# Optimization experiments

Hardware: AMD Instinct MI355X
Metric: run time of the kernel (lower is better)

Reference implementation:

```python
import jax, jax.numpy as jnp
import numpy as np

ALPHA = 0.25
GAMMA = 2.0
EPS = 1e-8
COST_CLASS_W = 1.0
COST_KP_W = 1.0


def setup_inputs() -> dict:
    key = jax.random.key(0)
    k1, k2, k3 = jax.random.split(key, 3)
    bs, nq, num_classes, T, D = 16, 1024, 2, 64, 63
    pred_logits = jax.random.normal(k1, (bs, nq, num_classes), dtype=jnp.float32)
    pred_keypoints = jax.random.normal(k2, (bs, nq, D), dtype=jnp.float32)
    tgt_kp = jax.random.normal(k3, (T, D), dtype=jnp.float32)  # ~half > 0 -> occlusion mask
    tgt_ids = jnp.ones((T,), dtype=jnp.int64)  # all 'hand' class; hand_idx all True
    return {"pred_logits": pred_logits, "pred_keypoints": pred_keypoints,
            "tgt_kp": tgt_kp, "tgt_ids": tgt_ids}


def reference(pred_logits, pred_keypoints, tgt_kp, tgt_ids):
    bs, nq, _ = pred_logits.shape
    out_prob = jax.nn.sigmoid(pred_logits.reshape(bs * nq, -1))   # [Q, C]
    out_kp = pred_keypoints.reshape(bs * nq, -1)                  # [Q, 63]

    # Focal-style classification cost
    neg = (1.0 - ALPHA) * out_prob ** GAMMA * (-jnp.log1p(-(out_prob - EPS) - 1.0 + 1.0) if False else -jnp.log(1.0 - out_prob + EPS))
    pos = ALPHA * (1.0 - out_prob) ** GAMMA * (-jnp.log(out_prob + EPS))
    cost_class = pos[:, tgt_ids] - neg[:, tgt_ids]                # [Q, T]

    # Masked L1 'cdist': only visible (tgt_kp > 0) coordinates contribute.
    occl_mask = (tgt_kp > 0).astype(out_kp.dtype)                 # [T, 63]
    diff = jnp.abs(out_kp[:, None, :] - tgt_kp[None, :, :])       # [Q, T, 63]
    cost_kp = jnp.sum(diff * occl_mask[None, :, :], axis=-1)      # [Q, T]

    C = COST_KP_W * cost_kp + COST_CLASS_W * cost_class
    return C.reshape(bs, nq, -1)  # [bs, nq, T]; CPU Hungarian (scipy) consumes per-sample blocks
```

## Files before the change

### kernel.cpp

```cpp
#include <hip/hip_runtime.h>


#define ALPHA 0.25f
#define EPS 1e-8f

constexpr int Q  = 16 * 1024;
constexpr int T  = 64;
constexpr int D  = 63;
constexpr int QB = 64;
constexpr int P  = 68;
constexpr int P2 = 34;

__device__ inline float focal_cost(float x) {
  float p   = 1.0f / (1.0f + __expf(-x));
  float pos = ALPHA * (1.0f - p) * (1.0f - p) * (-__logf(p + EPS));
  float neg = (1.0f - ALPHA) * p * p * (-__logf(1.0f - p + EPS));
  return pos - neg;
}

__global__ __launch_bounds__(512) void matcher_kernel(
    const float* __restrict__ logits,
    const float* __restrict__ kp,
    const float* __restrict__ tgt,
    const int*   __restrict__ ids,
    float* __restrict__ out)
{
  __shared__ __align__(16) float Bv[64 * P];
  __shared__ __align__(16) float Bm[64 * P];
  __shared__ float Lcc[QB * 2];
  __shared__ int   Ids[T];

  const int tid   = threadIdx.x;
  const int qbase = blockIdx.x * QB;

  {
    const float4* src = (const float4*)tgt;
    for (int j = tid; j < T * D / 4; j += 512) {
      float4 v = src[j];
      int i0 = 4 * j;
      float vv[4] = {v.x, v.y, v.z, v.w};
#pragma unroll
      for (int c = 0; c < 4; ++c) {
        int idx = i0 + c;
        int t = idx / D;
        int d = idx - t * D;
        Bv[d * P + t] = vv[c];
        Bm[d * P + t] = (vv[c] > 0.0f) ? 1.0f : 0.0f;
      }
    }
  }
  if (tid < QB * 2) Lcc[tid] = focal_cost(logits[qbase * 2 + tid]);
  if (tid < T) Ids[tid] = ids[tid];
  __syncthreads();

  const int qg = tid >> 5;
  const int tg = tid & 31;

  const float* __restrict__ r0 = kp + (qbase + qg * 4 + 0) * D;
  const float* __restrict__ r1 = kp + (qbase + qg * 4 + 1) * D;
  const float* __restrict__ r2 = kp + (qbase + qg * 4 + 2) * D;
  const float* __restrict__ r3 = kp + (qbase + qg * 4 + 3) * D;

  float2 acc0 = make_float2(0.f, 0.f);
  float2 acc1 = acc0, acc2 = acc0, acc3 = acc0;

  const float2* Bv2 = (const float2*)Bv;
  const float2* Bm2 = (const float2*)Bm;

#pragma unroll 7
  for (int d = 0; d < D; ++d) {
    float a0 = r0[d], a1 = r1[d], a2 = r2[d], a3 = r3[d];
    float2 bv = Bv2[d * P2 + tg];
    float2 bm = Bm2[d * P2 + tg];
    acc0.x += bm.x * fabsf(a0 - bv.x);
    acc0.y += bm.y * fabsf(a0 - bv.y);
    acc1.x += bm.x * fabsf(a1 - bv.x);
    acc1.y += bm.y * fabsf(a1 - bv.y);
    acc2.x += bm.x * fabsf(a2 - bv.x);
    acc2.y += bm.y * fabsf(a2 - bv.y);
    acc3.x += bm.x * fabsf(a3 - bv.x);
    acc3.y += bm.y * fabsf(a3 - bv.y);
  }

  const int t0 = tg * 2;
  int id0 = min(max(Ids[t0 + 0], 0), 1);
  int id1 = min(max(Ids[t0 + 1], 0), 1);

  float2 accs[4] = {acc0, acc1, acc2, acc3};
#pragma unroll
  for (int i = 0; i < 4; ++i) {
    int ql = qg * 4 + i;
    float cc[2] = {Lcc[ql * 2 + 0], Lcc[ql * 2 + 1]};
    float2 r;
    r.x = accs[i].x + cc[id0];
    r.y = accs[i].y + cc[id1];
    *(float2*)&out[(qbase + ql) * T + t0] = r;
  }
}

extern "C" void kernel_launch(void* const* d_in, const int* in_sizes, int n_in,
                              void* d_out, int out_size, void* d_ws, size_t ws_size,
                              hipStream_t stream) {
  const float* logits = (const float*)d_in[0];
  const float* kp     = (const float*)d_in[1];
  const float* tgt    = (const float*)d_in[2];
  const int*   ids    = (const int*)d_in[3];
  float* out = (float*)d_out;

  matcher_kernel<<<dim3(Q / QB), dim3(512), 0, stream>>>(logits, kp, tgt, ids, out);
}
```

Baseline: 70.63 us.

## Remap work to one target per lane with wave-uniform query rows

Each wave now handles four query rows, and each lane handles one target. The keypoint row index is made wave-uniform through readfirstlane, so those reads can become scalar loads. The separate occlusion-mask shared array is dropped and the mask is recomputed from the target value inside the loop. The query block shrinks from 64 to 32 rows, which doubles the number of blocks and adds per-block target staging, now done with a simpler transposed load.

New measurement: 67.28 us, median of 2. 1.05x faster.

```diff
diff --git a/kernel.cpp b/kernel.cpp
--- a/kernel.cpp
+++ b/kernel.cpp
@@ -7,9 +7,8 @@
 constexpr int Q  = 16 * 1024;
 constexpr int T  = 64;
 constexpr int D  = 63;
-constexpr int QB = 64;
-constexpr int P  = 68;
-constexpr int P2 = 34;
+constexpr int QB = 32;
+constexpr int P  = 66;
 
 __device__ inline float focal_cost(float x) {
   float p   = 1.0f / (1.0f + __expf(-x));
@@ -25,8 +24,7 @@
     const int*   __restrict__ ids,
     float* __restrict__ out)
 {
-  __shared__ __align__(16) float Bv[64 * P];
-  __shared__ __align__(16) float Bm[64 * P];
+  __shared__ __align__(16) float Bv[D * P];
   __shared__ float Lcc[QB * 2];
   __shared__ int   Ids[T];
 
@@ -34,68 +32,62 @@
   const int qbase = blockIdx.x * QB;
 
   {
-    const float4* src = (const float4*)tgt;
-    for (int j = tid; j < T * D / 4; j += 512) {
-      float4 v = src[j];
-      int i0 = 4 * j;
-      float vv[4] = {v.x, v.y, v.z, v.w};
+    const int t = tid >> 3;
+    const int c = tid & 7;
 #pragma unroll
-      for (int c = 0; c < 4; ++c) {
-        int idx = i0 + c;
-        int t = idx / D;
-        int d = idx - t * D;
-        Bv[d * P + t] = vv[c];
-        Bm[d * P + t] = (vv[c] > 0.0f) ? 1.0f : 0.0f;
-      }
+    for (int i = 0; i < 8; ++i) {
+      int d = 8 * c + i;
+      if (d < D) Bv[d * P + t] = tgt[t * D + d];
     }
   }
   if (tid < QB * 2) Lcc[tid] = focal_cost(logits[qbase * 2 + tid]);
   if (tid < T) Ids[tid] = ids[tid];
   __syncthreads();
 
-  const int qg = tid >> 5;
-  const int tg = tid & 31;
+  const int w    = __builtin_amdgcn_readfirstlane(tid) >> 6;
+  const int lane = tid & 63;
+  const int qrow = qbase + 4 * w;
 
-  const float* __restrict__ r0 = kp + (qbase + qg * 4 + 0) * D;
-  const float* __restrict__ r1 = kp + (qbase + qg * 4 + 1) * D;
-  const float* __restrict__ r2 = kp + (qbase + qg * 4 + 2) * D;
-  const float* __restrict__ r3 = kp + (qbase + qg * 4 + 3) * D;
+  const float* __restrict__ r0 = kp + (qrow + 0) * D;
+  const float* __restrict__ r1 = kp + (qrow + 1) * D;
+  const float* __restrict__ r2 = kp + (qrow + 2) * D;
+  const float* __restrict__ r3 = kp + (qrow + 3) * D;
 
-  float2 acc0 = make_float2(0.f, 0.f);
-  float2 acc1 = acc0, acc2 = acc0, acc3 = acc0;
+  float acc0 = 0.f, acc1 = 0.f, acc2 = 0.f, acc3 = 0.f;
 
-  const float2* Bv2 = (const float2*)Bv;
-  const float2* Bm2 = (const float2*)Bm;
-
-#pragma unroll 7
-  for (int d = 0; d < D; ++d) {
-    float a0 = r0[d], a1 = r1[d], a2 = r2[d], a3 = r3[d];
-    float2 bv = Bv2[d * P2 + tg];
-    float2 bm = Bm2[d * P2 + tg];
-    acc0.x += bm.x * fabsf(a0 - bv.x);
-    acc0.y += bm.y * fabsf(a0 - bv.y);
-    acc1.x += bm.x * fabsf(a1 - bv.x);
-    acc1.y += bm.y * fabsf(a1 - bv.y);
-    acc2.x += bm.x * fabsf(a2 - bv.x);
-    acc2.y += bm.y * fabsf(a2 - bv.y);
-    acc3.x += bm.x * fabsf(a3 - bv.x);
-    acc3.y += bm.y * fabsf(a3 - bv.y);
+#pragma unroll
+  for (int chunk = 0; chunk < 8; ++chunk) {
+    const int d0 = chunk * 8;
+    const int nd = (chunk == 7) ? 7 : 8;
+    float a0[8], a1[8], a2[8], a3[8];
+#pragma unroll
+    for (int j = 0; j < 8; ++j) {
+      if (j < nd) {
+        a0[j] = r0[d0 + j];
+        a1[j] = r1[d0 + j];
+        a2[j] = r2[d0 + j];
+        a3[j] = r3[d0 + j];
+      }
+    }
+#pragma unroll
+    for (int j = 0; j < 8; ++j) {
+      if (j < nd) {
+        float bv = Bv[(d0 + j) * P + lane];
+        float bm = bv > 0.0f ? 1.0f : 0.0f;
+        acc0 += bm * fabsf(a0[j] - bv);
+        acc1 += bm * fabsf(a1[j] - bv);
+        acc2 += bm * fabsf(a2[j] - bv);
+        acc3 += bm * fabsf(a3[j] - bv);
+      }
+    }
   }
 
-  const int t0 = tg * 2;
-  int id0 = min(max(Ids[t0 + 0], 0), 1);
-  int id1 = min(max(Ids[t0 + 1], 0), 1);
-
-  float2 accs[4] = {acc0, acc1, acc2, acc3};
-#pragma unroll
-  for (int i = 0; i < 4; ++i) {
-    int ql = qg * 4 + i;
-    float cc[2] = {Lcc[ql * 2 + 0], Lcc[ql * 2 + 1]};
-    float2 r;
-    r.x = accs[i].x + cc[id0];
-    r.y = accs[i].y + cc[id1];
-    *(float2*)&out[(qbase + ql) * T + t0] = r;
-  }
+  const int id = min(max(Ids[lane], 0), 1);
+  const int ql = 4 * w;
+  out[(qrow + 0) * T + lane] = acc0 + Lcc[(ql + 0) * 2 + id];
+  out[(qrow + 1) * T + lane] = acc1 + Lcc[(ql + 1) * 2 + id];
+  out[(qrow + 2) * T + lane] = acc2 + Lcc[(ql + 2) * 2 + id];
+  out[(qrow + 3) * T + lane] = acc3 + Lcc[(ql + 3) * 2 + id];
 }
 
 extern "C" void kernel_launch(void* const* d_in, const int* in_sizes, int n_in,
```
